# Kernel tuning notes

Hardware: AMD Instinct MI355X
Metric: run time of the kernel (lower is better)

Reference implementation:

```python
import jax, jax.numpy as jnp
import numpy as np

EMBED_DIM = 512
N_HEADS = 8
D_K = EMBED_DIM // N_HEADS

def _xavier(key, shape):
    fan_in, fan_out = shape[1], shape[0]
    limit = np.sqrt(6.0 / (fan_in + fan_out))
    return jax.random.uniform(key, shape, jnp.float32, -limit, limit)

def setup_inputs() -> dict:
    key = jax.random.key(0)
    ks = jax.random.split(key, 8)
    B, S, D = 2, 4096, EMBED_DIM
    return {
        "q": jax.random.normal(ks[0], (B, S, D), jnp.float32),
        "k": jax.random.normal(ks[1], (B, S, D), jnp.float32),
        "v": jax.random.normal(ks[2], (B, S, D), jnp.float32),
        "W_q": _xavier(ks[3], (D, D)),
        "W_k": _xavier(ks[4], (D, D)),
        "W_v": _xavier(ks[5], (D, D)),
        "W_o": _xavier(ks[6], (D, D)),
        "b_o": jnp.zeros((D,), jnp.float32),
    }

def reference(q, k, v, W_q, W_k, W_v, W_o, b_o):
    B, Sq, D = q.shape
    Sk = k.shape[1]
    # linear projections (torch Linear: x @ W.T)
    qh = (q @ W_q.T).reshape(B, Sq, N_HEADS, D_K).transpose(0, 2, 1, 3)
    kh = (k @ W_k.T).reshape(B, Sk, N_HEADS, D_K).transpose(0, 2, 1, 3)
    vh = (v @ W_v.T).reshape(B, Sk, N_HEADS, D_K).transpose(0, 2, 1, 3)
    scores = jnp.einsum('bhqd,bhkd->bhqk', qh, kh)  # [B,H,Sq,Sk]
    causal = jnp.triu(jnp.ones((Sq, Sk), bool), k=1)
    scores = jnp.where(causal, -jnp.inf, scores)
    attn = jax.nn.softmax(scores / np.sqrt(D_K), axis=-1)
    ctx = jnp.einsum('bhqk,bhkd->bhqd', attn, vh)
    ctx = ctx.transpose(0, 2, 1, 3).reshape(B, Sq, D)
    return ctx @ W_o.T + b_o
```

## Files before the change

kernel.cpp:

```cpp
#include <hip/hip_runtime.h>

typedef _Float16 f16;
typedef _Float16 f16x8 __attribute__((ext_vector_type(8)));
typedef _Float16 f16x4 __attribute__((ext_vector_type(4)));
typedef float f32x4 __attribute__((ext_vector_type(4)));

#define S_TOK 4096
#define NB 2
#define NH 8
#define DKH 64
#define DMODEL 512

static __device__ __forceinline__ f32x4 mfma16(f16x8 a, f16x8 b, f32x4 c) {
    return __builtin_amdgcn_mfma_f32_16x16x32_f16(a, b, c, 0, 0, 0);
}

__global__ __launch_bounds__(256)
void proj_fused_kernel(const float* __restrict__ qx, const float* __restrict__ kx,
                       const float* __restrict__ vx,
                       const float* __restrict__ Wqp, const float* __restrict__ Wkp,
                       const float* __restrict__ Wvp,
                       f16* __restrict__ qo, f16* __restrict__ ko, f16* __restrict__ vo)
{
    const int mode = blockIdx.z;
    const float* x = (mode == 0) ? qx : (mode == 1) ? kx : vx;
    const float* W = (mode == 0) ? Wqp : (mode == 1) ? Wkp : Wvp;
    f16* out = (mode == 0) ? qo : (mode == 1) ? ko : vo;

    __shared__ f16 As[128 * 40];
    __shared__ f16 Bs[128 * 40];
    const int m0 = blockIdx.x * 128;
    const int n0 = blockIdx.y * 128;
    const int tid = threadIdx.x;
    const int wv = tid >> 6;
    const int lane = tid & 63;
    const int lr = lane & 15, lg = lane >> 4;
    const int wm = (wv >> 1) * 64, wn = (wv & 1) * 64;

    f32x4 acc[4][4];
#pragma unroll
    for (int i = 0; i < 4; ++i)
#pragma unroll
        for (int j = 0; j < 4; ++j) acc[i][j] = f32x4{0.f, 0.f, 0.f, 0.f};

    for (int kb = 0; kb < DMODEL; kb += 32) {
#pragma unroll
        for (int c = 0; c < 2; ++c) {
            const int chunk = tid + c * 256;
            const int row = chunk >> 2;
            const int col = (chunk & 3) * 8;
            const float* ga = x + (size_t)(m0 + row) * DMODEL + kb + col;
            float4 a0 = *(const float4*)ga;
            float4 a1 = *(const float4*)(ga + 4);
            f16x8 ha = { (f16)a0.x, (f16)a0.y, (f16)a0.z, (f16)a0.w,
                         (f16)a1.x, (f16)a1.y, (f16)a1.z, (f16)a1.w };
            *(f16x8*)(As + row * 40 + col) = ha;
            const float* gb = W + (size_t)(n0 + row) * DMODEL + kb + col;
            float4 b0 = *(const float4*)gb;
            float4 b1 = *(const float4*)(gb + 4);
            f16x8 hb = { (f16)b0.x, (f16)b0.y, (f16)b0.z, (f16)b0.w,
                         (f16)b1.x, (f16)b1.y, (f16)b1.z, (f16)b1.w };
            *(f16x8*)(Bs + row * 40 + col) = hb;
        }
        __syncthreads();
        f16x8 af[4], bf[4];
#pragma unroll
        for (int i = 0; i < 4; ++i)
            af[i] = *(const f16x8*)(As + (wm + 16 * i + lr) * 40 + 8 * lg);
#pragma unroll
        for (int j = 0; j < 4; ++j)
            bf[j] = *(const f16x8*)(Bs + (wn + 16 * j + lr) * 40 + 8 * lg);
#pragma unroll
        for (int i = 0; i < 4; ++i)
#pragma unroll
            for (int j = 0; j < 4; ++j)
                acc[i][j] = mfma16(af[i], bf[j], acc[i][j]);
        __syncthreads();
    }

#pragma unroll
    for (int i = 0; i < 4; ++i) {
        const int mbase = m0 + wm + 16 * i + 4 * lg;
#pragma unroll
        for (int j = 0; j < 4; ++j) {
            const int n = n0 + wn + 16 * j + lr;
            const int h = n >> 6, dk = n & 63;
            if (mode == 2) {
                const int b = mbase >> 12;
                const int s = mbase & 4095;
                f16x4 v4;
#pragma unroll
                for (int r = 0; r < 4; ++r) v4[r] = (f16)acc[i][j][r];
                *(f16x4*)(out + ((size_t)(b * NH + h) * DKH + dk) * S_TOK + s) = v4;
            } else {
                const float sc = (mode == 0) ? 0.125f : 1.0f;
#pragma unroll
                for (int r = 0; r < 4; ++r) {
                    const int m = mbase + r;
                    const int b = m >> 12, s = m & 4095;
                    out[((size_t)(b * NH + h) * S_TOK + s) * DKH + dk] = (f16)(acc[i][j][r] * sc);
                }
            }
        }
    }
}

__global__ __launch_bounds__(512)
void attn_kernel(const f16* __restrict__ qh, const f16* __restrict__ kh,
                 const f16* __restrict__ vt, f16* __restrict__ ctx)
{
    __shared__ f16 Ks[2][64 * 64];
    __shared__ f16 Vs[2][64 * 64];
    __shared__ f16 Ps[8][16 * 72];

    const int bid = blockIdx.x;
    const int remap = (bid & 7) * 32 + (bid >> 3);
    const int bh = remap >> 4;
    const int pair = remap & 15;
    const int tid = threadIdx.x, wv = tid >> 6, lane = tid & 63;
    const int lr = lane & 15, lg = lane >> 4;

    const f16* Qp = qh + (size_t)bh * S_TOK * DKH;
    const f16* Kp = kh + (size_t)bh * S_TOK * DKH;
    const f16* Vp = vt + (size_t)bh * DKH * S_TOK;
    const int b = bh >> 3, h = bh & 7;

    const int srow = tid >> 3;
    const int sgr = (tid & 7) ^ (srow & 7);
    const f16* Kgb = Kp + srow * DKH + sgr * 8;
    const f16* Vgb = Vp + (size_t)srow * S_TOK + sgr * 8;
    const int ldst = srow * 64 + (tid & 7) * 8;
    f16* Pw = &Ps[wv][0];

    for (int seg = 0; seg < 2; ++seg) {
        const int qt = seg ? (31 - pair) : pair;
        const int q0 = qt * 128;
        const int nt = (q0 >> 6) + 2;
        const int qrow = q0 + 16 * wv + lr;

        f16x8 aq0 = *(const f16x8*)(Qp + (size_t)qrow * DKH + 8 * lg);
        f16x8 aq1 = *(const f16x8*)(Qp + (size_t)qrow * DKH + 32 + 8 * lg);

        f32x4 acco[4];
#pragma unroll
        for (int c = 0; c < 4; ++c) acco[c] = f32x4{0.f, 0.f, 0.f, 0.f};
        float mrow = -1e30f, lrow = 0.f;

        f16x8 kst = *(const f16x8*)Kgb;
        f16x8 vst = *(const f16x8*)Vgb;
        __syncthreads();
        *(f16x8*)(&Ks[0][ldst]) = kst;
        *(f16x8*)(&Vs[0][ldst]) = vst;

        int cur = 0;
        for (int t = 0; t < nt; ++t) {
            const bool pre = (t + 1 < nt);
            if (pre) {
                kst = *(const f16x8*)(Kgb + (size_t)(t + 1) * 64 * DKH);
                vst = *(const f16x8*)(Vgb + (t + 1) * 64);
            }
            __syncthreads();
            const f16* Kb = &Ks[cur][0];
            const f16* Vb = &Vs[cur][0];

            f32x4 sc[4];
#pragma unroll
            for (int c = 0; c < 4; ++c) {
                const int row = 16 * c + lr;
                const int rs = row & 7;
                f16x8 ak0 = *(const f16x8*)(Kb + row * 64 + ((lg ^ rs) * 8));
                f16x8 ak1 = *(const f16x8*)(Kb + row * 64 + (((lg + 4) ^ rs) * 8));
                sc[c] = mfma16(ak0, aq0, f32x4{0.f, 0.f, 0.f, 0.f});
                sc[c] = mfma16(ak1, aq1, sc[c]);
            }

            if (t >= nt - 2) {
#pragma unroll
                for (int c = 0; c < 4; ++c)
#pragma unroll
                    for (int r = 0; r < 4; ++r) {
                        const int kvg = t * 64 + 16 * c + 4 * lg + r;
                        sc[c][r] = (kvg > qrow) ? -1e30f : sc[c][r];
                    }
            }

            float tm = -1e30f;
#pragma unroll
            for (int c = 0; c < 4; ++c) {
                float m01 = fmaxf(fmaxf(sc[c][0], sc[c][1]), fmaxf(sc[c][2], sc[c][3]));
                tm = fmaxf(tm, m01);
            }
            tm = fmaxf(tm, __shfl_xor(tm, 16));
            tm = fmaxf(tm, __shfl_xor(tm, 32));
            const float mn = fmaxf(mrow, tm);
            const float sf = __expf(mrow - mn);
            float ts = 0.f;
            float pv[4][4];
#pragma unroll
            for (int c = 0; c < 4; ++c)
#pragma unroll
                for (int r = 0; r < 4; ++r) {
                    const float p = __expf(sc[c][r] - mn);
                    pv[c][r] = p;
                    ts += p;
                }
            ts += __shfl_xor(ts, 16);
            ts += __shfl_xor(ts, 32);
            lrow = lrow * sf + ts;
            mrow = mn;
#pragma unroll
            for (int c = 0; c < 4; ++c) acco[c] *= sf;

#pragma unroll
            for (int c = 0; c < 4; ++c) {
                f16x4 pk;
#pragma unroll
                for (int r = 0; r < 4; ++r) pk[r] = (f16)pv[c][r];
                *(f16x4*)(Pw + lr * 72 + 16 * c + 4 * lg) = pk;
            }
            f16x8 bp0 = *(const f16x8*)(Pw + lr * 72 + 8 * lg);
            f16x8 bp1 = *(const f16x8*)(Pw + lr * 72 + 32 + 8 * lg);

#pragma unroll
            for (int c = 0; c < 4; ++c) {
                const int row = 16 * c + lr;
                const int rs = row & 7;
                f16x8 av0 = *(const f16x8*)(Vb + row * 64 + ((lg ^ rs) * 8));
                f16x8 av1 = *(const f16x8*)(Vb + row * 64 + (((lg + 4) ^ rs) * 8));
                acco[c] = mfma16(av0, bp0, acco[c]);
                acco[c] = mfma16(av1, bp1, acco[c]);
            }

            if (pre) {
                *(f16x8*)(&Ks[cur ^ 1][ldst]) = kst;
                *(f16x8*)(&Vs[cur ^ 1][ldst]) = vst;
            }
            cur ^= 1;
        }

        const float invl = 1.0f / lrow;
        f16* cp = ctx + ((size_t)(b * S_TOK + qrow)) * DMODEL + h * DKH;
#pragma unroll
        for (int c = 0; c < 4; ++c) {
            f16x4 o;
#pragma unroll
            for (int r = 0; r < 4; ++r) o[r] = (f16)(acco[c][r] * invl);
            *(f16x4*)(cp + 16 * c + 4 * lg) = o;
        }
    }
}

__global__ __launch_bounds__(256)
void oproj_kernel(const f16* __restrict__ A, const float* __restrict__ W,
                  const float* __restrict__ bias, float* __restrict__ out)
{
    __shared__ f16 As[128 * 40];
    __shared__ f16 Bs[128 * 40];
    const int m0 = blockIdx.x * 128;
    const int n0 = blockIdx.y * 128;
    const int tid = threadIdx.x;
    const int wv = tid >> 6;
    const int lane = tid & 63;
    const int lr = lane & 15, lg = lane >> 4;
    const int wm = (wv >> 1) * 64, wn = (wv & 1) * 64;

    f32x4 acc[4][4];
#pragma unroll
    for (int i = 0; i < 4; ++i)
#pragma unroll
        for (int j = 0; j < 4; ++j) acc[i][j] = f32x4{0.f, 0.f, 0.f, 0.f};

    for (int kb = 0; kb < DMODEL; kb += 32) {
#pragma unroll
        for (int c = 0; c < 2; ++c) {
            const int chunk = tid + c * 256;
            const int row = chunk >> 2;
            const int col = (chunk & 3) * 8;
            *(f16x8*)(As + row * 40 + col) =
                *(const f16x8*)(A + (size_t)(m0 + row) * DMODEL + kb + col);
            const float* gb = W + (size_t)(n0 + row) * DMODEL + kb + col;
            float4 b0 = *(const float4*)gb;
            float4 b1 = *(const float4*)(gb + 4);
            f16x8 hb = { (f16)b0.x, (f16)b0.y, (f16)b0.z, (f16)b0.w,
                         (f16)b1.x, (f16)b1.y, (f16)b1.z, (f16)b1.w };
            *(f16x8*)(Bs + row * 40 + col) = hb;
        }
        __syncthreads();
        f16x8 af[4], bf[4];
#pragma unroll
        for (int i = 0; i < 4; ++i)
            af[i] = *(const f16x8*)(As + (wm + 16 * i + lr) * 40 + 8 * lg);
#pragma unroll
        for (int j = 0; j < 4; ++j)
            bf[j] = *(const f16x8*)(Bs + (wn + 16 * j + lr) * 40 + 8 * lg);
#pragma unroll
        for (int i = 0; i < 4; ++i)
#pragma unroll
            for (int j = 0; j < 4; ++j)
                acc[i][j] = mfma16(af[i], bf[j], acc[i][j]);
        __syncthreads();
    }

#pragma unroll
    for (int i = 0; i < 4; ++i) {
        const int mbase = m0 + wm + 16 * i + 4 * lg;
#pragma unroll
        for (int j = 0; j < 4; ++j) {
            const int n = n0 + wn + 16 * j + lr;
            const float bn = bias[n];
#pragma unroll
            for (int r = 0; r < 4; ++r) {
                const int m = mbase + r;
                out[(size_t)m * DMODEL + n] = acc[i][j][r] + bn;
            }
        }
    }
}

extern "C" void kernel_launch(void* const* d_in, const int* in_sizes, int n_in,
                              void* d_out, int out_size, void* d_ws, size_t ws_size,
                              hipStream_t stream) {
    const float* q  = (const float*)d_in[0];
    const float* k  = (const float*)d_in[1];
    const float* v  = (const float*)d_in[2];
    const float* Wq = (const float*)d_in[3];
    const float* Wk = (const float*)d_in[4];
    const float* Wv = (const float*)d_in[5];
    const float* Wo = (const float*)d_in[6];
    const float* bo = (const float*)d_in[7];
    float* out = (float*)d_out;

    const size_t per = (size_t)NB * NH * S_TOK * DKH;
    f16* qh  = (f16*)d_ws;
    f16* kh  = qh + per;
    f16* vt  = kh + per;
    f16* ctx = vt + per;

    proj_fused_kernel<<<dim3(64, 4, 3), 256, 0, stream>>>(q, k, v, Wq, Wk, Wv, qh, kh, vt);
    attn_kernel<<<dim3(256), 512, 0, stream>>>(qh, kh, vt, ctx);
    oproj_kernel<<<dim3(64, 4), 256, 0, stream>>>(ctx, Wo, bo, out);
}
```

Measured before the change: 125.0 us.

## Restructure attention: 32 query rows per wave, lazy rescale, exp2 softmax

Attention blocks shrink to 4 waves, each handling 32 query rows, so every K/V fragment read from shared memory feeds two MFMA tiles. The grid doubles to 512 blocks, one query tile per block, replacing the two-segment loop. The log2(e) factor is folded into the Q projection scale so softmax can use exp2f. The running-max rescale is skipped while the tile max stays within 8 of the current max. MFMA sections are wrapped in s_setprio. The cost is more registers per wave, and the lazy rescale lets fp16 P values reach about 256.

```diff
diff --git a/kernel.cpp b/kernel.cpp
--- a/kernel.cpp
+++ b/kernel.cpp
@@ -93,7 +93,7 @@
                 for (int r = 0; r < 4; ++r) v4[r] = (f16)acc[i][j][r];
                 *(f16x4*)(out + ((size_t)(b * NH + h) * DKH + dk) * S_TOK + s) = v4;
             } else {
-                const float sc = (mode == 0) ? 0.125f : 1.0f;
+                const float sc = (mode == 0) ? 0.1803368801111244f : 1.0f;
 #pragma unroll
                 for (int r = 0; r < 4; ++r) {
                     const int m = mbase + r;
@@ -105,18 +105,22 @@
     }
 }
 
-__global__ __launch_bounds__(512)
+__global__ __launch_bounds__(256)
 void attn_kernel(const f16* __restrict__ qh, const f16* __restrict__ kh,
                  const f16* __restrict__ vt, f16* __restrict__ ctx)
 {
     __shared__ f16 Ks[2][64 * 64];
     __shared__ f16 Vs[2][64 * 64];
-    __shared__ f16 Ps[8][16 * 72];
+    __shared__ f16 Ps[4][32 * 72];
 
     const int bid = blockIdx.x;
-    const int remap = (bid & 7) * 32 + (bid >> 3);
-    const int bh = remap >> 4;
-    const int pair = remap & 15;
+    const int xc = bid & 7, w = bid >> 3;
+    const int bh = 2 * xc + (w & 1);
+    const int qi = (w >> 1) & 15;
+    const int qt = (w >> 5) ? (31 - qi) : qi;
+    const int q0 = qt * 128;
+    const int nt = 2 * qt + 2;
+
     const int tid = threadIdx.x, wv = tid >> 6, lane = tid & 63;
     const int lr = lane & 15, lg = lane >> 4;
 
@@ -125,126 +129,158 @@
     const f16* Vp = vt + (size_t)bh * DKH * S_TOK;
     const int b = bh >> 3, h = bh & 7;
 
-    const int srow = tid >> 3;
-    const int sgr = (tid & 7) ^ (srow & 7);
-    const f16* Kgb = Kp + srow * DKH + sgr * 8;
-    const f16* Vgb = Vp + (size_t)srow * S_TOK + sgr * 8;
-    const int ldst = srow * 64 + (tid & 7) * 8;
+    const int srow0 = tid >> 3;
+    const int sg = tid & 7;
+    const int sgx = sg ^ (srow0 & 7);
+    const f16* Kg = Kp + srow0 * DKH + sgx * 8;
+    const f16* Vg = Vp + (size_t)srow0 * S_TOK + sgx * 8;
+    const int ld0 = srow0 * 64 + sg * 8;
     f16* Pw = &Ps[wv][0];
 
-    for (int seg = 0; seg < 2; ++seg) {
-        const int qt = seg ? (31 - pair) : pair;
-        const int q0 = qt * 128;
-        const int nt = (q0 >> 6) + 2;
-        const int qrow = q0 + 16 * wv + lr;
-
-        f16x8 aq0 = *(const f16x8*)(Qp + (size_t)qrow * DKH + 8 * lg);
-        f16x8 aq1 = *(const f16x8*)(Qp + (size_t)qrow * DKH + 32 + 8 * lg);
-
-        f32x4 acco[4];
-#pragma unroll
-        for (int c = 0; c < 4; ++c) acco[c] = f32x4{0.f, 0.f, 0.f, 0.f};
-        float mrow = -1e30f, lrow = 0.f;
-
-        f16x8 kst = *(const f16x8*)Kgb;
-        f16x8 vst = *(const f16x8*)Vgb;
-        __syncthreads();
-        *(f16x8*)(&Ks[0][ldst]) = kst;
-        *(f16x8*)(&Vs[0][ldst]) = vst;
-
-        int cur = 0;
-        for (int t = 0; t < nt; ++t) {
-            const bool pre = (t + 1 < nt);
-            if (pre) {
-                kst = *(const f16x8*)(Kgb + (size_t)(t + 1) * 64 * DKH);
-                vst = *(const f16x8*)(Vgb + (t + 1) * 64);
-            }
-            __syncthreads();
-            const f16* Kb = &Ks[cur][0];
-            const f16* Vb = &Vs[cur][0];
-
-            f32x4 sc[4];
-#pragma unroll
-            for (int c = 0; c < 4; ++c) {
-                const int row = 16 * c + lr;
-                const int rs = row & 7;
-                f16x8 ak0 = *(const f16x8*)(Kb + row * 64 + ((lg ^ rs) * 8));
-                f16x8 ak1 = *(const f16x8*)(Kb + row * 64 + (((lg + 4) ^ rs) * 8));
-                sc[c] = mfma16(ak0, aq0, f32x4{0.f, 0.f, 0.f, 0.f});
-                sc[c] = mfma16(ak1, aq1, sc[c]);
-            }
-
-            if (t >= nt - 2) {
-#pragma unroll
-                for (int c = 0; c < 4; ++c)
+    const int qc0 = q0 + 32 * wv + lr;
+    f16x8 aq[2][2];
+#pragma unroll
+    for (int u = 0; u < 2; ++u)
+#pragma unroll
+        for (int kk = 0; kk < 2; ++kk)
+            aq[u][kk] = *(const f16x8*)(Qp + (size_t)(qc0 + 16 * u) * DKH + 32 * kk + 8 * lg);
+
+    f32x4 acco[4][2];
+#pragma unroll
+    for (int c = 0; c < 4; ++c)
+#pragma unroll
+        for (int u = 0; u < 2; ++u) acco[c][u] = f32x4{0.f, 0.f, 0.f, 0.f};
+    float mrow[2] = { -1e30f, -1e30f };
+    float lrow[2] = { 0.f, 0.f };
+
+    f16x8 k0a = *(const f16x8*)(Kg);
+    f16x8 k0b = *(const f16x8*)(Kg + 32 * DKH);
+    f16x8 v0a = *(const f16x8*)(Vg);
+    f16x8 v0b = *(const f16x8*)(Vg + 32 * S_TOK);
+    *(f16x8*)(&Ks[0][ld0]) = k0a;  *(f16x8*)(&Ks[0][ld0 + 2048]) = k0b;
+    *(f16x8*)(&Vs[0][ld0]) = v0a;  *(f16x8*)(&Vs[0][ld0 + 2048]) = v0b;
+
+    int cur = 0;
+    for (int t = 0; t < nt; ++t) {
+        const bool pre = (t + 1 < nt);
+        f16x8 kna, knb, vna, vnb;
+        if (pre) {
+            const int kvn = (t + 1) * 64;
+            kna = *(const f16x8*)(Kg + (size_t)kvn * DKH);
+            knb = *(const f16x8*)(Kg + (size_t)(kvn + 32) * DKH);
+            vna = *(const f16x8*)(Vg + kvn);
+            vnb = *(const f16x8*)(Vg + (size_t)32 * S_TOK + kvn);
+        }
+        __syncthreads();
+        const f16* Kb = &Ks[cur][0];
+        const f16* Vb = &Vs[cur][0];
+
+        f32x4 sc[4][2];
+        __builtin_amdgcn_s_setprio(1);
+#pragma unroll
+        for (int c = 0; c < 4; ++c) {
+            const int row = 16 * c + lr;
+            const int rs = row & 7;
+            f16x8 ak0 = *(const f16x8*)(Kb + row * 64 + ((lg ^ rs) * 8));
+            f16x8 ak1 = *(const f16x8*)(Kb + row * 64 + (((lg + 4) ^ rs) * 8));
+            sc[c][0] = mfma16(ak0, aq[0][0], f32x4{0.f, 0.f, 0.f, 0.f});
+            sc[c][0] = mfma16(ak1, aq[0][1], sc[c][0]);
+            sc[c][1] = mfma16(ak0, aq[1][0], f32x4{0.f, 0.f, 0.f, 0.f});
+            sc[c][1] = mfma16(ak1, aq[1][1], sc[c][1]);
+        }
+        __builtin_amdgcn_s_setprio(0);
+
+        if (t >= nt - 2) {
+#pragma unroll
+            for (int c = 0; c < 4; ++c)
+#pragma unroll
+                for (int u = 0; u < 2; ++u)
 #pragma unroll
                     for (int r = 0; r < 4; ++r) {
                         const int kvg = t * 64 + 16 * c + 4 * lg + r;
-                        sc[c][r] = (kvg > qrow) ? -1e30f : sc[c][r];
+                        sc[c][u][r] = (kvg > qc0 + 16 * u) ? -1e30f : sc[c][u][r];
                     }
+        }
+
+        float tm[2];
+#pragma unroll
+        for (int u = 0; u < 2; ++u) {
+            float a0 = fmaxf(fmaxf(sc[0][u][0], sc[0][u][1]), fmaxf(sc[0][u][2], sc[0][u][3]));
+            float a1 = fmaxf(fmaxf(sc[1][u][0], sc[1][u][1]), fmaxf(sc[1][u][2], sc[1][u][3]));
+            float a2 = fmaxf(fmaxf(sc[2][u][0], sc[2][u][1]), fmaxf(sc[2][u][2], sc[2][u][3]));
+            float a3 = fmaxf(fmaxf(sc[3][u][0], sc[3][u][1]), fmaxf(sc[3][u][2], sc[3][u][3]));
+            float v = fmaxf(fmaxf(a0, a1), fmaxf(a2, a3));
+            v = fmaxf(v, __shfl_xor(v, 16));
+            v = fmaxf(v, __shfl_xor(v, 32));
+            tm[u] = v;
+        }
+        const int okd = (tm[0] <= mrow[0] + 8.f) && (tm[1] <= mrow[1] + 8.f);
+        if (!__all(okd)) {
+#pragma unroll
+            for (int u = 0; u < 2; ++u) {
+                const float mn = fmaxf(mrow[u], tm[u]);
+                const float sf = exp2f(mrow[u] - mn);
+                lrow[u] *= sf;
+                mrow[u] = mn;
+#pragma unroll
+                for (int c = 0; c < 4; ++c) acco[c][u] *= sf;
             }
-
-            float tm = -1e30f;
+        }
+#pragma unroll
+        for (int u = 0; u < 2; ++u) {
+            float ts = 0.f;
 #pragma unroll
             for (int c = 0; c < 4; ++c) {
-                float m01 = fmaxf(fmaxf(sc[c][0], sc[c][1]), fmaxf(sc[c][2], sc[c][3]));
-                tm = fmaxf(tm, m01);
+                f16x4 pk;
+#pragma unroll
+                for (int r = 0; r < 4; ++r) {
+                    const float p = exp2f(sc[c][u][r] - mrow[u]);
+                    ts += p;
+                    pk[r] = (f16)p;
+                }
+                *(f16x4*)(Pw + (16 * u + lr) * 72 + 16 * c + 4 * lg) = pk;
             }
-            tm = fmaxf(tm, __shfl_xor(tm, 16));
-            tm = fmaxf(tm, __shfl_xor(tm, 32));
-            const float mn = fmaxf(mrow, tm);
-            const float sf = __expf(mrow - mn);
-            float ts = 0.f;
-            float pv[4][4];
-#pragma unroll
-            for (int c = 0; c < 4; ++c)
-#pragma unroll
-                for (int r = 0; r < 4; ++r) {
-                    const float p = __expf(sc[c][r] - mn);
-                    pv[c][r] = p;
-                    ts += p;
-                }
             ts += __shfl_xor(ts, 16);
             ts += __shfl_xor(ts, 32);
-            lrow = lrow * sf + ts;
-            mrow = mn;
-#pragma unroll
-            for (int c = 0; c < 4; ++c) acco[c] *= sf;
-
-#pragma unroll
-            for (int c = 0; c < 4; ++c) {
-                f16x4 pk;
-#pragma unroll
-                for (int r = 0; r < 4; ++r) pk[r] = (f16)pv[c][r];
-                *(f16x4*)(Pw + lr * 72 + 16 * c + 4 * lg) = pk;
-            }
-            f16x8 bp0 = *(const f16x8*)(Pw + lr * 72 + 8 * lg);
-            f16x8 bp1 = *(const f16x8*)(Pw + lr * 72 + 32 + 8 * lg);
-
-#pragma unroll
-            for (int c = 0; c < 4; ++c) {
-                const int row = 16 * c + lr;
-                const int rs = row & 7;
-                f16x8 av0 = *(const f16x8*)(Vb + row * 64 + ((lg ^ rs) * 8));
-                f16x8 av1 = *(const f16x8*)(Vb + row * 64 + (((lg + 4) ^ rs) * 8));
-                acco[c] = mfma16(av0, bp0, acco[c]);
-                acco[c] = mfma16(av1, bp1, acco[c]);
-            }
-
-            if (pre) {
-                *(f16x8*)(&Ks[cur ^ 1][ldst]) = kst;
-                *(f16x8*)(&Vs[cur ^ 1][ldst]) = vst;
-            }
-            cur ^= 1;
-        }
-
-        const float invl = 1.0f / lrow;
-        f16* cp = ctx + ((size_t)(b * S_TOK + qrow)) * DMODEL + h * DKH;
+            lrow[u] += ts;
+        }
+
+        f16x8 bp[2][2];
+#pragma unroll
+        for (int u = 0; u < 2; ++u)
+#pragma unroll
+            for (int kk = 0; kk < 2; ++kk)
+                bp[u][kk] = *(const f16x8*)(Pw + (16 * u + lr) * 72 + 32 * kk + 8 * lg);
+        __builtin_amdgcn_s_setprio(1);
+#pragma unroll
+        for (int c = 0; c < 4; ++c) {
+            const int row = 16 * c + lr;
+            const int rs = row & 7;
+            f16x8 av0 = *(const f16x8*)(Vb + row * 64 + ((lg ^ rs) * 8));
+            f16x8 av1 = *(const f16x8*)(Vb + row * 64 + (((lg + 4) ^ rs) * 8));
+            acco[c][0] = mfma16(av0, bp[0][0], acco[c][0]);
+            acco[c][0] = mfma16(av1, bp[0][1], acco[c][0]);
+            acco[c][1] = mfma16(av0, bp[1][0], acco[c][1]);
+            acco[c][1] = mfma16(av1, bp[1][1], acco[c][1]);
+        }
+        __builtin_amdgcn_s_setprio(0);
+
+        if (pre) {
+            *(f16x8*)(&Ks[cur ^ 1][ld0]) = kna;  *(f16x8*)(&Ks[cur ^ 1][ld0 + 2048]) = knb;
+            *(f16x8*)(&Vs[cur ^ 1][ld0]) = vna;  *(f16x8*)(&Vs[cur ^ 1][ld0 + 2048]) = vnb;
+        }
+        cur ^= 1;
+    }
+
+#pragma unroll
+    for (int u = 0; u < 2; ++u) {
+        const float invl = 1.0f / lrow[u];
+        f16* cp = ctx + ((size_t)(b * S_TOK + qc0 + 16 * u)) * DMODEL + h * DKH;
 #pragma unroll
         for (int c = 0; c < 4; ++c) {
             f16x4 o;
 #pragma unroll
-            for (int r = 0; r < 4; ++r) o[r] = (f16)(acco[c][r] * invl);
+            for (int r = 0; r < 4; ++r) o[r] = (f16)(acco[c][u][r] * invl);
             *(f16x4*)(cp + 16 * c + 4 * lg) = o;
         }
     }
@@ -337,6 +373,6 @@
     f16* ctx = vt + per;
 
     proj_fused_kernel<<<dim3(64, 4, 3), 256, 0, stream>>>(q, k, v, Wq, Wk, Wv, qh, kh, vt);
-    attn_kernel<<<dim3(256), 512, 0, stream>>>(qh, kh, vt, ctx);
+    attn_kernel<<<dim3(512), 256, 0, stream>>>(qh, kh, vt, ctx);
     oproj_kernel<<<dim3(64, 4), 256, 0, stream>>>(ctx, Wo, bo, out);
 }
```

Result: slower. 156.7 us (+25.4%).

## Split causal attention KV range across blocks with 32x32 MFMA and log-sum-exp merge

Applied to the files above, without the earlier changes.

Attention is restructured so each block handles a query tile with its KV range split into two balanced halves. Partial outputs and log-sum-exp values go to workspace, and a new merge kernel combines them. The inner loop moves to 32x32x16 MFMA with 4 waves of 32 query rows each. It uses exp2 with log2(e) folded into the Q scale and skips the rescale when the running max grows by less than a threshold. This adds an extra kernel launch and workspace traffic in exchange for better load balance and more blocks in flight.

```diff
diff --git a/kernel.cpp b/kernel.cpp
--- a/kernel.cpp
+++ b/kernel.cpp
@@ -4,6 +4,7 @@
 typedef _Float16 f16x8 __attribute__((ext_vector_type(8)));
 typedef _Float16 f16x4 __attribute__((ext_vector_type(4)));
 typedef float f32x4 __attribute__((ext_vector_type(4)));
+typedef float f32x16 __attribute__((ext_vector_type(16)));
 
 #define S_TOK 4096
 #define NB 2
@@ -13,6 +14,9 @@
 
 static __device__ __forceinline__ f32x4 mfma16(f16x8 a, f16x8 b, f32x4 c) {
     return __builtin_amdgcn_mfma_f32_16x16x32_f16(a, b, c, 0, 0, 0);
+}
+static __device__ __forceinline__ f32x16 mfma32(f16x8 a, f16x8 b, f32x16 c) {
+    return __builtin_amdgcn_mfma_f32_32x32x16_f16(a, b, c, 0, 0, 0);
 }
 
 __global__ __launch_bounds__(256)
@@ -93,7 +97,7 @@
                 for (int r = 0; r < 4; ++r) v4[r] = (f16)acc[i][j][r];
                 *(f16x4*)(out + ((size_t)(b * NH + h) * DKH + dk) * S_TOK + s) = v4;
             } else {
-                const float sc = (mode == 0) ? 0.125f : 1.0f;
+                const float sc = (mode == 0) ? 0.1803368801111244f : 1.0f;
 #pragma unroll
                 for (int r = 0; r < 4; ++r) {
                     const int m = mbase + r;
@@ -105,149 +109,183 @@
     }
 }
 
-__global__ __launch_bounds__(512)
+__global__ __launch_bounds__(256, 3)
 void attn_kernel(const f16* __restrict__ qh, const f16* __restrict__ kh,
-                 const f16* __restrict__ vt, f16* __restrict__ ctx)
+                 const f16* __restrict__ vt, f16* __restrict__ pO, float* __restrict__ pL)
 {
     __shared__ f16 Ks[2][64 * 64];
     __shared__ f16 Vs[2][64 * 64];
-    __shared__ f16 Ps[8][16 * 72];
+    __shared__ f16 Ps[4][32 * 72];
 
     const int bid = blockIdx.x;
-    const int remap = (bid & 7) * 32 + (bid >> 3);
-    const int bh = remap >> 4;
-    const int pair = remap & 15;
+    const int bh = 2 * (bid & 7) + ((bid >> 3) & 1);
+    const int j = bid >> 4;
     const int tid = threadIdx.x, wv = tid >> 6, lane = tid & 63;
-    const int lr = lane & 15, lg = lane >> 4;
+    const int l31 = lane & 31, h = lane >> 5;
 
     const f16* Qp = qh + (size_t)bh * S_TOK * DKH;
     const f16* Kp = kh + (size_t)bh * S_TOK * DKH;
     const f16* Vp = vt + (size_t)bh * DKH * S_TOK;
-    const int b = bh >> 3, h = bh & 7;
-
-    const int srow = tid >> 3;
-    const int sgr = (tid & 7) ^ (srow & 7);
-    const f16* Kgb = Kp + srow * DKH + sgr * 8;
-    const f16* Vgb = Vp + (size_t)srow * S_TOK + sgr * 8;
-    const int ldst = srow * 64 + (tid & 7) * 8;
+
+    const int srow = tid >> 2;
+    const int s0 = (tid & 3) + 4 * ((tid >> 2) & 1);
+    const int s1 = s0 ^ 4;
+    const int g0 = s0 ^ (srow & 7), g1 = s1 ^ (srow & 7);
+    const int ldA = srow * 64 + s0 * 8, ldB = srow * 64 + s1 * 8;
     f16* Pw = &Ps[wv][0];
 
     for (int seg = 0; seg < 2; ++seg) {
-        const int qt = seg ? (31 - pair) : pair;
+        const int qt = seg ? (31 - j) : j;
+        const int t0 = seg ? (qt + 1) : 0;
+        const int t1 = seg ? (2 * qt + 2) : (j + 1);
         const int q0 = qt * 128;
-        const int nt = (q0 >> 6) + 2;
-        const int qrow = q0 + 16 * wv + lr;
-
-        f16x8 aq0 = *(const f16x8*)(Qp + (size_t)qrow * DKH + 8 * lg);
-        f16x8 aq1 = *(const f16x8*)(Qp + (size_t)qrow * DKH + 32 + 8 * lg);
-
-        f32x4 acco[4];
-#pragma unroll
-        for (int c = 0; c < 4; ++c) acco[c] = f32x4{0.f, 0.f, 0.f, 0.f};
-        float mrow = -1e30f, lrow = 0.f;
-
-        f16x8 kst = *(const f16x8*)Kgb;
-        f16x8 vst = *(const f16x8*)Vgb;
-        __syncthreads();
-        *(f16x8*)(&Ks[0][ldst]) = kst;
-        *(f16x8*)(&Vs[0][ldst]) = vst;
+        const int qw = q0 + 32 * wv + l31;
+        const int unit = (bh * 32 + qt) * 2 + seg;
+
+        f16x8 aq[4];
+#pragma unroll
+        for (int s = 0; s < 4; ++s)
+            aq[s] = *(const f16x8*)(Qp + (size_t)qw * DKH + 16 * s + 8 * h);
+
+        f32x16 accO0 = {}, accO1 = {};
+        float mrow = -1e20f, lrow = 0.f;
+
+        f16x8 ka = *(const f16x8*)(Kp + (size_t)(64 * t0 + srow) * DKH + g0 * 8);
+        f16x8 kb = *(const f16x8*)(Kp + (size_t)(64 * t0 + srow) * DKH + g1 * 8);
+        f16x8 va = *(const f16x8*)(Vp + (size_t)srow * S_TOK + 64 * t0 + g0 * 8);
+        f16x8 vb = *(const f16x8*)(Vp + (size_t)srow * S_TOK + 64 * t0 + g1 * 8);
+        __syncthreads();
+        *(f16x8*)(&Ks[0][ldA]) = ka;  *(f16x8*)(&Ks[0][ldB]) = kb;
+        *(f16x8*)(&Vs[0][ldA]) = va;  *(f16x8*)(&Vs[0][ldB]) = vb;
 
         int cur = 0;
-        for (int t = 0; t < nt; ++t) {
-            const bool pre = (t + 1 < nt);
+        for (int t = t0; t < t1; ++t) {
+            const bool pre = (t + 1 < t1);
+            f16x8 kna, knb, vna, vnb;
             if (pre) {
-                kst = *(const f16x8*)(Kgb + (size_t)(t + 1) * 64 * DKH);
-                vst = *(const f16x8*)(Vgb + (t + 1) * 64);
+                kna = *(const f16x8*)(Kp + (size_t)(64 * (t + 1) + srow) * DKH + g0 * 8);
+                knb = *(const f16x8*)(Kp + (size_t)(64 * (t + 1) + srow) * DKH + g1 * 8);
+                vna = *(const f16x8*)(Vp + (size_t)srow * S_TOK + 64 * (t + 1) + g0 * 8);
+                vnb = *(const f16x8*)(Vp + (size_t)srow * S_TOK + 64 * (t + 1) + g1 * 8);
             }
             __syncthreads();
             const f16* Kb = &Ks[cur][0];
             const f16* Vb = &Vs[cur][0];
 
-            f32x4 sc[4];
-#pragma unroll
-            for (int c = 0; c < 4; ++c) {
-                const int row = 16 * c + lr;
-                const int rs = row & 7;
-                f16x8 ak0 = *(const f16x8*)(Kb + row * 64 + ((lg ^ rs) * 8));
-                f16x8 ak1 = *(const f16x8*)(Kb + row * 64 + (((lg + 4) ^ rs) * 8));
-                sc[c] = mfma16(ak0, aq0, f32x4{0.f, 0.f, 0.f, 0.f});
-                sc[c] = mfma16(ak1, aq1, sc[c]);
-            }
-
-            if (t >= nt - 2) {
-#pragma unroll
-                for (int c = 0; c < 4; ++c)
-#pragma unroll
-                    for (int r = 0; r < 4; ++r) {
-                        const int kvg = t * 64 + 16 * c + 4 * lg + r;
-                        sc[c][r] = (kvg > qrow) ? -1e30f : sc[c][r];
-                    }
+            f32x16 accS0 = {}, accS1 = {};
+            __builtin_amdgcn_s_setprio(1);
+#pragma unroll
+            for (int s = 0; s < 4; ++s) {
+                f16x8 ak0 = *(const f16x8*)(Kb + (l31) * 64 + ((2 * s + h) ^ (l31 & 7)) * 8);
+                f16x8 ak1 = *(const f16x8*)(Kb + (32 + l31) * 64 + ((2 * s + h) ^ (l31 & 7)) * 8);
+                accS0 = mfma32(ak0, aq[s], accS0);
+                accS1 = mfma32(ak1, aq[s], accS1);
+            }
+            __builtin_amdgcn_s_setprio(0);
+
+            if (t >= 2 * qt) {
+#pragma unroll
+                for (int e = 0; e < 16; ++e) {
+                    const int kvb = 64 * t + (e & 3) + 8 * (e >> 2) + 4 * h;
+                    accS0[e] = (kvb > qw) ? -1e30f : accS0[e];
+                    accS1[e] = (kvb + 32 > qw) ? -1e30f : accS1[e];
+                }
             }
 
             float tm = -1e30f;
 #pragma unroll
-            for (int c = 0; c < 4; ++c) {
-                float m01 = fmaxf(fmaxf(sc[c][0], sc[c][1]), fmaxf(sc[c][2], sc[c][3]));
-                tm = fmaxf(tm, m01);
-            }
-            tm = fmaxf(tm, __shfl_xor(tm, 16));
+            for (int e = 0; e < 16; ++e) tm = fmaxf(tm, fmaxf(accS0[e], accS1[e]));
             tm = fmaxf(tm, __shfl_xor(tm, 32));
-            const float mn = fmaxf(mrow, tm);
-            const float sf = __expf(mrow - mn);
+            if (!__all(tm <= mrow + 8.f)) {
+                const float mn = fmaxf(mrow, tm);
+                const float sf = exp2f(mrow - mn);
+                lrow *= sf;
+                accO0 *= sf;  accO1 *= sf;
+                mrow = mn;
+            }
             float ts = 0.f;
-            float pv[4][4];
-#pragma unroll
-            for (int c = 0; c < 4; ++c)
+#pragma unroll
+            for (int g = 0; g < 4; ++g) {
+                f16x4 u, u2;
 #pragma unroll
                 for (int r = 0; r < 4; ++r) {
-                    const float p = __expf(sc[c][r] - mn);
-                    pv[c][r] = p;
+                    const float p = exp2f(accS0[4 * g + r] - mrow);
                     ts += p;
+                    u[r] = (f16)p;
+                    const float pq = exp2f(accS1[4 * g + r] - mrow);
+                    ts += pq;
+                    u2[r] = (f16)pq;
                 }
-            ts += __shfl_xor(ts, 16);
+                *(f16x4*)(Pw + l31 * 72 + 8 * g + 4 * h) = u;
+                *(f16x4*)(Pw + l31 * 72 + 32 + 8 * g + 4 * h) = u2;
+            }
             ts += __shfl_xor(ts, 32);
-            lrow = lrow * sf + ts;
-            mrow = mn;
-#pragma unroll
-            for (int c = 0; c < 4; ++c) acco[c] *= sf;
-
-#pragma unroll
-            for (int c = 0; c < 4; ++c) {
-                f16x4 pk;
-#pragma unroll
-                for (int r = 0; r < 4; ++r) pk[r] = (f16)pv[c][r];
-                *(f16x4*)(Pw + lr * 72 + 16 * c + 4 * lg) = pk;
-            }
-            f16x8 bp0 = *(const f16x8*)(Pw + lr * 72 + 8 * lg);
-            f16x8 bp1 = *(const f16x8*)(Pw + lr * 72 + 32 + 8 * lg);
-
-#pragma unroll
-            for (int c = 0; c < 4; ++c) {
-                const int row = 16 * c + lr;
-                const int rs = row & 7;
-                f16x8 av0 = *(const f16x8*)(Vb + row * 64 + ((lg ^ rs) * 8));
-                f16x8 av1 = *(const f16x8*)(Vb + row * 64 + (((lg + 4) ^ rs) * 8));
-                acco[c] = mfma16(av0, bp0, acco[c]);
-                acco[c] = mfma16(av1, bp1, acco[c]);
-            }
+            lrow += ts;
+
+            __builtin_amdgcn_s_setprio(1);
+#pragma unroll
+            for (int s = 0; s < 4; ++s) {
+                f16x8 bp = *(const f16x8*)(Pw + l31 * 72 + 16 * s + 8 * h);
+                f16x8 av0 = *(const f16x8*)(Vb + (l31) * 64 + ((2 * s + h) ^ (l31 & 7)) * 8);
+                f16x8 av1 = *(const f16x8*)(Vb + (32 + l31) * 64 + ((2 * s + h) ^ (l31 & 7)) * 8);
+                accO0 = mfma32(av0, bp, accO0);
+                accO1 = mfma32(av1, bp, accO1);
+            }
+            __builtin_amdgcn_s_setprio(0);
 
             if (pre) {
-                *(f16x8*)(&Ks[cur ^ 1][ldst]) = kst;
-                *(f16x8*)(&Vs[cur ^ 1][ldst]) = vst;
+                *(f16x8*)(&Ks[cur ^ 1][ldA]) = kna;  *(f16x8*)(&Ks[cur ^ 1][ldB]) = knb;
+                *(f16x8*)(&Vs[cur ^ 1][ldA]) = vna;  *(f16x8*)(&Vs[cur ^ 1][ldB]) = vnb;
             }
             cur ^= 1;
         }
 
-        const float invl = 1.0f / lrow;
-        f16* cp = ctx + ((size_t)(b * S_TOK + qrow)) * DMODEL + h * DKH;
-#pragma unroll
-        for (int c = 0; c < 4; ++c) {
-            f16x4 o;
-#pragma unroll
-            for (int r = 0; r < 4; ++r) o[r] = (f16)(acco[c][r] * invl);
-            *(f16x4*)(cp + 16 * c + 4 * lg) = o;
-        }
-    }
+        const float invl = (lrow > 0.f) ? (1.f / lrow) : 0.f;
+        f16* Ob = pO + ((size_t)unit * 128 + (32 * wv + l31)) * DKH;
+#pragma unroll
+        for (int g = 0; g < 4; ++g) {
+            f16x4 o0, o1;
+#pragma unroll
+            for (int r = 0; r < 4; ++r) {
+                o0[r] = (f16)(accO0[4 * g + r] * invl);
+                o1[r] = (f16)(accO1[4 * g + r] * invl);
+            }
+            *(f16x4*)(Ob + 8 * g + 4 * h) = o0;
+            *(f16x4*)(Ob + 32 + 8 * g + 4 * h) = o1;
+        }
+        if (h == 0)
+            pL[unit * 128 + 32 * wv + l31] =
+                (lrow > 0.f) ? (mrow + __log2f(lrow)) : -1e30f;
+    }
+}
+
+__global__ __launch_bounds__(256)
+void merge_kernel(const f16* __restrict__ pO, const float* __restrict__ pL,
+                  f16* __restrict__ ctx)
+{
+    const int tid = threadIdx.x;
+    const int R = blockIdx.x * 32 + (tid >> 3);
+    const int dkg = tid & 7;
+    const int bh = R >> 12, q = R & 4095;
+    const int qt = q >> 7, qi = q & 127;
+    const int u0 = (bh * 32 + qt) * 2, u1 = u0 + 1;
+
+    const float L0 = pL[u0 * 128 + qi];
+    const float L1 = pL[u1 * 128 + qi];
+    const float Lm = fmaxf(L0, L1);
+    const float w0 = exp2f(L0 - Lm);
+    const float w1 = exp2f(L1 - Lm);
+    const float inv = 1.f / (w0 + w1);
+
+    f16x8 a = *(const f16x8*)(pO + ((size_t)u0 * 128 + qi) * DKH + dkg * 8);
+    f16x8 b = *(const f16x8*)(pO + ((size_t)u1 * 128 + qi) * DKH + dkg * 8);
+    f16x8 o;
+#pragma unroll
+    for (int i = 0; i < 8; ++i)
+        o[i] = (f16)((w0 * (float)a[i] + w1 * (float)b[i]) * inv);
+
+    const int bb = bh >> 3, hh = bh & 7;
+    *(f16x8*)(ctx + ((size_t)(bb * S_TOK + q)) * DMODEL + hh * DKH + dkg * 8) = o;
 }
 
 __global__ __launch_bounds__(256)
@@ -335,8 +373,11 @@
     f16* kh  = qh + per;
     f16* vt  = kh + per;
     f16* ctx = vt + per;
+    f16* pO  = ctx + per;
+    float* pL = (float*)(pO + (size_t)1024 * 128 * 64);
 
     proj_fused_kernel<<<dim3(64, 4, 3), 256, 0, stream>>>(q, k, v, Wq, Wk, Wv, qh, kh, vt);
-    attn_kernel<<<dim3(256), 512, 0, stream>>>(qh, kh, vt, ctx);
+    attn_kernel<<<dim3(512), 256, 0, stream>>>(qh, kh, vt, pO, pL);
+    merge_kernel<<<dim3(2048), 256, 0, stream>>>(pO, pL, ctx);
     oproj_kernel<<<dim3(64, 4), 256, 0, stream>>>(ctx, Wo, bo, out);
 }
```

After: 132.7 us. 1.06x slower.
